# Kernel tuning notes

Hardware: AMD Instinct MI355X
Metric: run time of the kernel (lower is better)

The kernel has to match this reference:

```python
import jax, jax.numpy as jnp
import numpy as np
import math

B, C, H, W = 4, 256, 64, 64
NUM_HEADS = 4
GROUPS = 32
EPS = 1e-5


def setup_inputs() -> dict:
    key = jax.random.key(0)
    ks = jax.random.split(key, 7)
    x = jax.random.normal(ks[0], (B, C, H, W), dtype=jnp.float32)
    gn_w = jax.random.normal(ks[1], (C,), dtype=jnp.float32) * 0.02 + 1.0
    gn_b = jax.random.normal(ks[2], (C,), dtype=jnp.float32) * 0.02
    qkv_w = jax.random.normal(ks[3], (3 * C, C), dtype=jnp.float32) * (1.0 / math.sqrt(C))
    qkv_b = jax.random.normal(ks[4], (3 * C,), dtype=jnp.float32) * 0.02
    proj_w = jax.random.normal(ks[5], (C, C), dtype=jnp.float32) * (1.0 / math.sqrt(C))
    proj_b = jax.random.normal(ks[6], (C,), dtype=jnp.float32) * 0.02
    return {"x": x, "gn_w": gn_w, "gn_b": gn_b, "qkv_w": qkv_w,
            "qkv_b": qkv_b, "proj_w": proj_w, "proj_b": proj_b}


def reference(x, gn_w, gn_b, qkv_w, qkv_b, proj_w, proj_b):
    b, c, h, w = x.shape
    t = h * w
    xf = x.reshape(b, c, t)                       # [B, C, T]

    # GroupNorm(32, C) over (channels-in-group, T)
    xg = xf.reshape(b, GROUPS, c // GROUPS, t)
    mean = jnp.mean(xg, axis=(2, 3), keepdims=True)
    var = jnp.var(xg, axis=(2, 3), keepdims=True)
    xn = ((xg - mean) * jax.lax.rsqrt(var + EPS)).reshape(b, c, t)
    xn = xn * gn_w[None, :, None] + gn_b[None, :, None]

    # 1x1 conv QKV: [B, 3C, T]
    qkv = jnp.einsum('oc,bct->bot', qkv_w, xn) + qkv_b[None, :, None]

    nh = NUM_HEADS
    ch = c // nh
    q, k, v = jnp.split(qkv, 3, axis=1)           # each [B, H*ch, T]
    q = q.reshape(b * nh, ch, t)
    k = k.reshape(b * nh, ch, t)
    v = v.reshape(b * nh, ch, t)

    scale = 1.0 / math.sqrt(math.sqrt(ch))
    logits = jnp.einsum('bct,bcs->bts', q * scale, k * scale)   # [B*H, T, T]
    weight = jax.nn.softmax(logits.astype(jnp.float32), axis=-1).astype(logits.dtype)
    a = jnp.einsum('bts,bcs->bct', weight, v)     # [B*H, ch, T]
    a = a.reshape(b, c, t)

    hproj = jnp.einsum('oc,bct->bot', proj_w, a) + proj_b[None, :, None]
    return (xf + hproj).reshape(b, c, h, w)
```

## Files before the change

### kernel.cpp

```cpp
#include <hip/hip_runtime.h>
#include <cstdint>
#include <cstddef>

#define TT 4096
#define CCH 256

typedef __attribute__((ext_vector_type(8))) short short8;
typedef __attribute__((ext_vector_type(4))) float f32x4;
typedef __attribute__((ext_vector_type(4))) unsigned int u32x4;

__device__ __forceinline__ unsigned short f2bf(float f){
  unsigned int x = __float_as_uint(f);
  x += 0x7fffu + ((x >> 16) & 1u);
  return (unsigned short)(x >> 16);
}
__device__ __forceinline__ int sw(int row, int col){
  return (row << 6) + ((((col >> 3) ^ (row & 7)) << 3)) + (col & 7);
}
__device__ __forceinline__ void pl16(unsigned &a, unsigned &b){
  asm("v_permlane16_swap_b32 %0, %1" : "+v"(a), "+v"(b));
}
__device__ __forceinline__ void pl32(unsigned &a, unsigned &b){
  asm("v_permlane32_swap_b32 %0, %1" : "+v"(a), "+v"(b));
}
__device__ __forceinline__ unsigned cvt_pk_bf16(float lo, float hi){
  unsigned r;
  asm("v_cvt_pk_bf16_f32 %0, %1, %2" : "=v"(r) : "v"(lo), "v"(hi));
  return r;
}

__global__ __launch_bounds__(256)
void wconv_gn(const float* __restrict__ qkv_w, const float* __restrict__ proj_w,
              const float* __restrict__ x,
              unsigned short* __restrict__ wq_bf, unsigned short* __restrict__ wp_bf,
              float* __restrict__ stats){
  int bid = blockIdx.x, tid = threadIdx.x;
  if (bid < 256){
    const float* src = (bid < 192) ? qkv_w : proj_w;
    unsigned short* dst = (bid < 192) ? wq_bf : wp_bf;
    int i = (bid < 192 ? bid : bid - 192) * 256 + tid;
    float4 u = *(const float4*)(src + (size_t)i * 4);
    ushort4 r; r.x = f2bf(u.x); r.y = f2bf(u.y); r.z = f2bf(u.z); r.w = f2bf(u.w);
    *(ushort4*)(dst + (size_t)i * 4) = r;
    return;
  }
  int sg = bid - 256;
  const float4* p = (const float4*)(x + (size_t)sg * 32768);
  float s = 0.f, sq = 0.f;
  #pragma unroll
  for (int it = 0; it < 32; ++it){
    float4 u = p[it * 256 + tid];
    s  += u.x + u.y + u.z + u.w;
    sq += u.x*u.x + u.y*u.y + u.z*u.z + u.w*u.w;
  }
  #pragma unroll
  for (int off = 32; off >= 1; off >>= 1){
    s  += __shfl_down(s, off);
    sq += __shfl_down(sq, off);
  }
  __shared__ float ls[4], lq[4];
  int w_ = tid >> 6, lane = tid & 63;
  if (lane == 0){ ls[w_] = s; lq[w_] = sq; }
  __syncthreads();
  if (tid == 0){
    float S = ls[0]+ls[1]+ls[2]+ls[3];
    float Q = lq[0]+lq[1]+lq[2]+lq[3];
    float mean = S * (1.f/32768.f);
    float var  = Q * (1.f/32768.f) - mean*mean;
    stats[2*sg]   = mean;
    stats[2*sg+1] = rsqrtf(var + 1e-5f);
  }
}

__global__ __launch_bounds__(256)
void gn_apply_t(const float* __restrict__ x, const float* __restrict__ gw,
                const float* __restrict__ gb, const float* __restrict__ stats,
                unsigned short* __restrict__ xnT){
  __shared__ unsigned short t_lds[64][72];
  int tid = threadIdx.x;
  int t0 = blockIdx.x << 6, c0 = blockIdx.y << 6, b = blockIdx.z;
  int t4 = (tid & 15) << 2, cr = tid >> 4;
  #pragma unroll
  for (int pass = 0; pass < 4; ++pass){
    int cl = (pass << 4) + cr;
    int c = c0 + cl;
    int sg = (b << 5) | (c >> 3);
    float mean = stats[2*sg], rstd = stats[2*sg+1];
    float sc = gw[c] * rstd;
    float sh = gb[c] - mean * sc;
    float4 u = *(const float4*)(x + ((size_t)(b*CCH + c))*TT + t0 + t4);
    t_lds[t4+0][cl] = f2bf(u.x*sc + sh);
    t_lds[t4+1][cl] = f2bf(u.y*sc + sh);
    t_lds[t4+2][cl] = f2bf(u.z*sc + sh);
    t_lds[t4+3][cl] = f2bf(u.w*sc + sh);
  }
  __syncthreads();
  #pragma unroll
  for (int pass = 0; pass < 2; ++pass){
    int chunk = (pass << 8) + tid;
    int row = chunk >> 3, c8 = (chunk & 7) << 3;
    *(uint4*)(xnT + ((size_t)b*TT + t0 + row)*256 + c0 + c8) = *(const uint4*)&t_lds[row][c8];
  }
}

__global__ __launch_bounds__(256)
void qkv_mfma(const unsigned short* __restrict__ wb, const float* __restrict__ bias,
              const unsigned short* __restrict__ xnT,
              unsigned short* __restrict__ qT, unsigned short* __restrict__ kT,
              unsigned short* __restrict__ vO){
  __shared__ unsigned short x_lds[4096];
  int tid = threadIdx.x;
  int w = tid >> 6, lane = tid & 63, quad = lane >> 4, l15 = lane & 15;
  int t0 = blockIdx.x << 6, o0 = blockIdx.y << 6, b = blockIdx.z;
  const unsigned short* xb = xnT + (size_t)b * TT * 256;
  const unsigned short* wrow = wb + (size_t)(o0 + (w << 4) + l15) * 256;
  f32x4 acc[4];
  #pragma unroll
  for (int nt = 0; nt < 4; ++nt) acc[nt] = (f32x4){0.f,0.f,0.f,0.f};
  for (int ks = 0; ks < 4; ++ks){
    int k0 = ks << 6;
    __syncthreads();
    #pragma unroll
    for (int pass = 0; pass < 2; ++pass){
      int chunk = (pass << 8) + tid;
      int row = chunk >> 3, c8 = (chunk & 7) << 3;
      *(uint4*)&x_lds[sw(row, c8)] = *(const uint4*)(xb + (size_t)(t0 + row)*256 + k0 + c8);
    }
    __syncthreads();
    short8 wa0 = *(const short8*)(wrow + k0 + (quad << 3));
    short8 wa1 = *(const short8*)(wrow + k0 + 32 + (quad << 3));
    #pragma unroll
    for (int nt = 0; nt < 4; ++nt){
      short8 xb0 = *(const short8*)&x_lds[sw((nt << 4) + l15, quad << 3)];
      short8 xb1 = *(const short8*)&x_lds[sw((nt << 4) + l15, 32 + (quad << 3))];
      acc[nt] = __builtin_amdgcn_mfma_f32_16x16x32_bf16(wa0, xb0, acc[nt], 0, 0, 0);
      acc[nt] = __builtin_amdgcn_mfma_f32_16x16x32_bf16(wa1, xb1, acc[nt], 0, 0, 0);
    }
  }
  int sec = blockIdx.y >> 2, h = blockIdx.y & 3, bh = (b << 2) | h;
  float bs[4];
  #pragma unroll
  for (int r = 0; r < 4; ++r) bs[r] = bias[o0 + (w << 4) + (quad << 2) + r];
  __syncthreads();
  if (sec < 2){
    float qsc = (sec == 0) ? 0.125f * 1.44269504f : 1.0f;
    #pragma unroll
    for (int nt = 0; nt < 4; ++nt){
      ushort4 pk;
      pk.x = f2bf((acc[nt][0] + bs[0]) * qsc);
      pk.y = f2bf((acc[nt][1] + bs[1]) * qsc);
      pk.z = f2bf((acc[nt][2] + bs[2]) * qsc);
      pk.w = f2bf((acc[nt][3] + bs[3]) * qsc);
      *(ushort4*)&x_lds[sw((nt << 4) + l15, (w << 4) + (quad << 2))] = pk;
    }
    __syncthreads();
    unsigned short* dst = (sec == 0) ? qT : kT;
    #pragma unroll
    for (int pass = 0; pass < 2; ++pass){
      int chunk = (pass << 8) + tid;
      int row = chunk >> 3, c8 = (chunk & 7) << 3;
      *(uint4*)(dst + ((size_t)bh*TT + t0 + row)*64 + c8) = *(const uint4*)&x_lds[sw(row, c8)];
    }
  } else {
    #pragma unroll
    for (int nt = 0; nt < 4; ++nt)
      #pragma unroll
      for (int r = 0; r < 4; ++r)
        x_lds[sw((w << 4) + (quad << 2) + r, (nt << 4) + l15)] = f2bf(acc[nt][r] + bs[r]);
    __syncthreads();
    #pragma unroll
    for (int pass = 0; pass < 2; ++pass){
      int chunk = (pass << 8) + tid;
      int row = chunk >> 3, c8 = (chunk & 7) << 3;
      *(uint4*)(vO + ((size_t)bh*64 + row)*TT + t0 + c8) = *(const uint4*)&x_lds[sw(row, c8)];
    }
  }
}

__global__ __launch_bounds__(256, 4)
void attn10(const unsigned short* __restrict__ qT, const unsigned short* __restrict__ kT,
            const unsigned short* __restrict__ vO,
            float* __restrict__ oP, float* __restrict__ lP){
  __shared__ __align__(16) unsigned short k_lds[4096];
  __shared__ __align__(16) unsigned short v_lds[4096];
  int tid = threadIdx.x;
  int w = tid >> 6, lane = tid & 63, quad = lane >> 4, l15 = lane & 15;
  int bh = blockIdx.x & 15;
  int sh = (blockIdx.x >> 4) & 1;
  int tb = blockIdx.x >> 5;
  int t0 = tb << 7;
  const unsigned short* qg = qT + (size_t)bh * TT * 64;
  const unsigned short* kg = kT + (size_t)bh * TT * 64;
  const unsigned short* vg = vO + (size_t)bh * 64 * TT;
  int sbase = sh << 11;

  int row0 = tid >> 3, c80 = (tid & 7) << 3;
  int row1 = row0 + 32;
  int soff0 = sw(row0, c80), soff1 = sw(row1, c80);

  short8 qf[2][2];
  #pragma unroll
  for (int tt2 = 0; tt2 < 2; ++tt2)
    #pragma unroll
    for (int h = 0; h < 2; ++h)
      qf[tt2][h] = *(const short8*)(qg + (size_t)(t0 + (w<<5) + (tt2<<4) + l15)*64 + (h<<5) + (quad<<3));

  short8 ones;
  #pragma unroll
  for (int i = 0; i < 8; ++i) ones[i] = (short)0x3F80;

  f32x4 o_acc[2][4];
  #pragma unroll
  for (int tt2 = 0; tt2 < 2; ++tt2)
    #pragma unroll
    for (int ct = 0; ct < 4; ++ct) o_acc[tt2][ct] = (f32x4){0.f,0.f,0.f,0.f};
  float l_[2] = {0.f, 0.f};

  uint4 kr0 = *(const uint4*)(kg + (size_t)(sbase + row0)*64 + c80);
  uint4 kr1 = *(const uint4*)(kg + (size_t)(sbase + row1)*64 + c80);
  uint4 vr0 = *(const uint4*)(vg + (size_t)row0*TT + sbase + c80);
  uint4 vr1 = *(const uint4*)(vg + (size_t)row1*TT + sbase + c80);

  for (int st = 0; st < 32; ++st){
    __syncthreads();
    *(uint4*)&k_lds[soff0] = kr0;
    *(uint4*)&k_lds[soff1] = kr1;
    *(uint4*)&v_lds[soff0] = vr0;
    *(uint4*)&v_lds[soff1] = vr1;
    if (st < 31){
      int sn = sbase + ((st + 1) << 6);
      kr0 = *(const uint4*)(kg + (size_t)(sn + row0)*64 + c80);
      kr1 = *(const uint4*)(kg + (size_t)(sn + row1)*64 + c80);
      vr0 = *(const uint4*)(vg + (size_t)row0*TT + sn + c80);
      vr1 = *(const uint4*)(vg + (size_t)row1*TT + sn + c80);
    }
    __syncthreads();
    short8 pb[2][2];
    __builtin_amdgcn_s_setprio(1);
    #pragma unroll
    for (int h = 0; h < 2; ++h){
      short8 kae0 = *(const short8*)&k_lds[sw((h << 5) + l15, quad << 3)];
      short8 kae1 = *(const short8*)&k_lds[sw((h << 5) + l15, 32 + (quad << 3))];
      short8 kao0 = *(const short8*)&k_lds[sw((h << 5) + 16 + l15, quad << 3)];
      short8 kao1 = *(const short8*)&k_lds[sw((h << 5) + 16 + l15, 32 + (quad << 3))];
      #pragma unroll
      for (int tt2 = 0; tt2 < 2; ++tt2){
        f32x4 ze = (f32x4){-16.f, -16.f, -16.f, -16.f};
        f32x4 zo = ze;
        ze = __builtin_amdgcn_mfma_f32_16x16x32_bf16(kae0, qf[tt2][0], ze, 0, 0, 0);
        ze = __builtin_amdgcn_mfma_f32_16x16x32_bf16(kae1, qf[tt2][1], ze, 0, 0, 0);
        zo = __builtin_amdgcn_mfma_f32_16x16x32_bf16(kao0, qf[tt2][0], zo, 0, 0, 0);
        zo = __builtin_amdgcn_mfma_f32_16x16x32_bf16(kao1, qf[tt2][1], zo, 0, 0, 0);
        unsigned A0 = cvt_pk_bf16(exp2f(ze[0]), exp2f(ze[1]));
        unsigned A1 = cvt_pk_bf16(exp2f(ze[2]), exp2f(ze[3]));
        unsigned B0 = cvt_pk_bf16(exp2f(zo[0]), exp2f(zo[1]));
        unsigned B1 = cvt_pk_bf16(exp2f(zo[2]), exp2f(zo[3]));
        pl32(A0, B0); pl16(A0, B0);
        pl32(A1, B1); pl16(A1, B1);
        union { u32x4 u; short8 s; } pu;
        pu.u = (u32x4){A0, A1, B0, B1};
        pb[tt2][h] = pu.s;
      }
    }
    #pragma unroll
    for (int tt2 = 0; tt2 < 2; ++tt2){
      f32x4 ls4 = (f32x4){0.f,0.f,0.f,0.f};
      ls4 = __builtin_amdgcn_mfma_f32_16x16x32_bf16(ones, pb[tt2][0], ls4, 0, 0, 0);
      ls4 = __builtin_amdgcn_mfma_f32_16x16x32_bf16(ones, pb[tt2][1], ls4, 0, 0, 0);
      l_[tt2] += ls4[0];
    }
    #pragma unroll
    for (int ct = 0; ct < 4; ++ct){
      short8 va0 = *(const short8*)&v_lds[sw((ct << 4) + l15, quad << 3)];
      short8 va1 = *(const short8*)&v_lds[sw((ct << 4) + l15, 32 + (quad << 3))];
      #pragma unroll
      for (int tt2 = 0; tt2 < 2; ++tt2){
        o_acc[tt2][ct] = __builtin_amdgcn_mfma_f32_16x16x32_bf16(va0, pb[tt2][0], o_acc[tt2][ct], 0, 0, 0);
        o_acc[tt2][ct] = __builtin_amdgcn_mfma_f32_16x16x32_bf16(va1, pb[tt2][1], o_acc[tt2][ct], 0, 0, 0);
      }
    }
    __builtin_amdgcn_s_setprio(0);
  }
  int bid2 = (tb << 4) | bh;
  size_t fb = (size_t)sh * (512*8192) + (size_t)bid2 * 8192;
  #pragma unroll
  for (int tt2 = 0; tt2 < 2; ++tt2)
    #pragma unroll
    for (int ct = 0; ct < 4; ++ct)
      *(f32x4*)(oP + fb + (size_t)((((tt2 << 2) + ct) << 8) + tid) * 4) = o_acc[tt2][ct];
  if (quad == 0){
    #pragma unroll
    for (int tt2 = 0; tt2 < 2; ++tt2)
      lP[((sh << 4) + bh) * 4096 + t0 + (w << 5) + (tt2 << 4) + l15] = l_[tt2];
  }
}

__global__ __launch_bounds__(256)
void attn_comb(const float* __restrict__ oP, const float* __restrict__ lP,
               unsigned short* __restrict__ aT){
  __shared__ __align__(16) unsigned short p_lds[8192];
  int tid = threadIdx.x;
  int w = tid >> 6, lane = tid & 63, quad = lane >> 4, l15 = lane & 15;
  int bh = blockIdx.x & 15, tb = blockIdx.x >> 4;
  int t0 = tb << 7;
  size_t fb = (size_t)blockIdx.x * 8192;
  const size_t HALF = (size_t)512 * 8192;
  float ir[2];
  #pragma unroll
  for (int tt2 = 0; tt2 < 2; ++tt2){
    int t = t0 + (w << 5) + (tt2 << 4) + l15;
    ir[tt2] = 1.f / (lP[bh*4096 + t] + lP[(16 + bh)*4096 + t]);
  }
  #pragma unroll
  for (int tt2 = 0; tt2 < 2; ++tt2)
    #pragma unroll
    for (int ct = 0; ct < 4; ++ct){
      size_t off = fb + (size_t)((((tt2 << 2) + ct) << 8) + tid) * 4;
      f32x4 a = *(const f32x4*)(oP + off);
      f32x4 b = *(const f32x4*)(oP + HALF + off);
      ushort4 ok;
      ok.x = f2bf((a[0] + b[0]) * ir[tt2]);
      ok.y = f2bf((a[1] + b[1]) * ir[tt2]);
      ok.z = f2bf((a[2] + b[2]) * ir[tt2]);
      ok.w = f2bf((a[3] + b[3]) * ir[tt2]);
      *(ushort4*)&p_lds[sw((w << 5) + (tt2 << 4) + l15, (ct << 4) + (quad << 2))] = ok;
    }
  __syncthreads();
  size_t abase = ((size_t)(bh >> 2)*TT + t0)*256 + (size_t)(bh & 3)*64;
  #pragma unroll
  for (int pass = 0; pass < 4; ++pass){
    int chunk = (pass << 8) + tid;
    int row = chunk >> 3, c8 = (chunk & 7) << 3;
    *(uint4*)(aT + abase + (size_t)row*256 + c8) = *(const uint4*)&p_lds[sw(row, c8)];
  }
}

__global__ __launch_bounds__(256)
void proj_mfma(const unsigned short* __restrict__ wb, const float* __restrict__ bias,
               const unsigned short* __restrict__ aT, const float* __restrict__ x,
               float* __restrict__ out){
  __shared__ unsigned short x_lds[4096];
  int tid = threadIdx.x;
  int w = tid >> 6, lane = tid & 63, quad = lane >> 4, l15 = lane & 15;
  int t0 = blockIdx.x << 6, o0 = blockIdx.y << 6, b = blockIdx.z;
  const unsigned short* xb = aT + (size_t)b * TT * 256;
  const unsigned short* wrow = wb + (size_t)(o0 + (w << 4) + l15) * 256;
  f32x4 acc[4];
  #pragma unroll
  for (int nt = 0; nt < 4; ++nt) acc[nt] = (f32x4){0.f,0.f,0.f,0.f};
  for (int ks = 0; ks < 4; ++ks){
    int k0 = ks << 6;
    __syncthreads();
    #pragma unroll
    for (int pass = 0; pass < 2; ++pass){
      int chunk = (pass << 8) + tid;
      int row = chunk >> 3, c8 = (chunk & 7) << 3;
      *(uint4*)&x_lds[sw(row, c8)] = *(const uint4*)(xb + (size_t)(t0 + row)*256 + k0 + c8);
    }
    __syncthreads();
    short8 wa0 = *(const short8*)(wrow + k0 + (quad << 3));
    short8 wa1 = *(const short8*)(wrow + k0 + 32 + (quad << 3));
    #pragma unroll
    for (int nt = 0; nt < 4; ++nt){
      short8 xb0 = *(const short8*)&x_lds[sw((nt << 4) + l15, quad << 3)];
      short8 xb1 = *(const short8*)&x_lds[sw((nt << 4) + l15, 32 + (quad << 3))];
      acc[nt] = __builtin_amdgcn_mfma_f32_16x16x32_bf16(wa0, xb0, acc[nt], 0, 0, 0);
      acc[nt] = __builtin_amdgcn_mfma_f32_16x16x32_bf16(wa1, xb1, acc[nt], 0, 0, 0);
    }
  }
  #pragma unroll
  for (int r = 0; r < 4; ++r){
    int o = o0 + (w << 4) + (quad << 2) + r;
    float bsv = bias[o];
    #pragma unroll
    for (int nt = 0; nt < 4; ++nt){
      size_t idx = ((size_t)(b*CCH + o))*TT + t0 + (nt << 4) + l15;
      out[idx] = acc[nt][r] + bsv + x[idx];
    }
  }
}

extern "C" void kernel_launch(void* const* d_in, const int* in_sizes, int n_in,
                              void* d_out, int out_size, void* d_ws, size_t ws_size,
                              hipStream_t stream){
  const float* x      = (const float*)d_in[0];
  const float* gn_w   = (const float*)d_in[1];
  const float* gn_b   = (const float*)d_in[2];
  const float* qkv_w  = (const float*)d_in[3];
  const float* qkv_b  = (const float*)d_in[4];
  const float* proj_w = (const float*)d_in[5];
  const float* proj_b = (const float*)d_in[6];
  float* out = (float*)d_out;

  float* stats = (float*)d_ws;
  unsigned short* wq_bf = (unsigned short*)(stats + 1024);
  unsigned short* wp_bf = wq_bf + (size_t)768*256;
  unsigned short* xnT   = wp_bf + (size_t)256*256;
  unsigned short* qT    = xnT + (size_t)4*TT*256;
  unsigned short* kT    = qT  + (size_t)16*TT*64;
  unsigned short* vO    = kT  + (size_t)16*TT*64;
  unsigned short* aT    = vO  + (size_t)16*64*TT;
  float* oP = (float*)(aT + (size_t)16*64*TT);
  float* lP = oP + (size_t)2*512*8192;

  wconv_gn<<<384, 256, 0, stream>>>(qkv_w, proj_w, x, wq_bf, wp_bf, stats);
  gn_apply_t<<<dim3(64, 4, 4), 256, 0, stream>>>(x, gn_w, gn_b, stats, xnT);
  qkv_mfma<<<dim3(64, 12, 4), 256, 0, stream>>>(wq_bf, qkv_b, xnT, qT, kT, vO);
  attn10<<<1024, 256, 0, stream>>>(qT, kT, vO, oP, lP);
  attn_comb<<<512, 256, 0, stream>>>(oP, lP, aT);
  proj_mfma<<<dim3(64, 4, 4), 256, 0, stream>>>(wp_bf, proj_b, aT, x, out);
}
```

Measured before the change: 209.9 us.

## Split attention keys four ways with bf16 partial outputs

The attention kernel now splits the key sequence into four chunks instead of two, doubling the grid to 2048 blocks and halving each block's loop length. It also asks for higher occupancy in the launch bounds. Partial outputs are stored as bf16 instead of fp32, which holds total partial-buffer traffic roughly constant, and the combine kernel sums four partials. The trade-off is more precision loss in the partials and a tighter register budget that could cause spills.

```diff
diff --git a/kernel.cpp b/kernel.cpp
--- a/kernel.cpp
+++ b/kernel.cpp
@@ -13,6 +13,9 @@
   unsigned int x = __float_as_uint(f);
   x += 0x7fffu + ((x >> 16) & 1u);
   return (unsigned short)(x >> 16);
+}
+__device__ __forceinline__ float bf2f(unsigned short u){
+  union { unsigned int i; float f; } v; v.i = ((unsigned int)u) << 16; return v.f;
 }
 __device__ __forceinline__ int sw(int row, int col){
   return (row << 6) + ((((col >> 3) ^ (row & 7)) << 3)) + (col & 7);
@@ -177,22 +180,22 @@
   }
 }
 
-__global__ __launch_bounds__(256, 4)
+__global__ __launch_bounds__(256, 8)
 void attn10(const unsigned short* __restrict__ qT, const unsigned short* __restrict__ kT,
             const unsigned short* __restrict__ vO,
-            float* __restrict__ oP, float* __restrict__ lP){
+            unsigned short* __restrict__ oPb, float* __restrict__ lP){
   __shared__ __align__(16) unsigned short k_lds[4096];
   __shared__ __align__(16) unsigned short v_lds[4096];
   int tid = threadIdx.x;
   int w = tid >> 6, lane = tid & 63, quad = lane >> 4, l15 = lane & 15;
   int bh = blockIdx.x & 15;
-  int sh = (blockIdx.x >> 4) & 1;
-  int tb = blockIdx.x >> 5;
+  int sh = (blockIdx.x >> 4) & 3;
+  int tb = blockIdx.x >> 6;
   int t0 = tb << 7;
   const unsigned short* qg = qT + (size_t)bh * TT * 64;
   const unsigned short* kg = kT + (size_t)bh * TT * 64;
   const unsigned short* vg = vO + (size_t)bh * 64 * TT;
-  int sbase = sh << 11;
+  int sbase = sh << 10;
 
   int row0 = tid >> 3, c80 = (tid & 7) << 3;
   int row1 = row0 + 32;
@@ -221,13 +224,13 @@
   uint4 vr0 = *(const uint4*)(vg + (size_t)row0*TT + sbase + c80);
   uint4 vr1 = *(const uint4*)(vg + (size_t)row1*TT + sbase + c80);
 
-  for (int st = 0; st < 32; ++st){
+  for (int st = 0; st < 16; ++st){
     __syncthreads();
     *(uint4*)&k_lds[soff0] = kr0;
     *(uint4*)&k_lds[soff1] = kr1;
     *(uint4*)&v_lds[soff0] = vr0;
     *(uint4*)&v_lds[soff1] = vr1;
-    if (st < 31){
+    if (st < 15){
       int sn = sbase + ((st + 1) << 6);
       kr0 = *(const uint4*)(kg + (size_t)(sn + row0)*64 + c80);
       kr1 = *(const uint4*)(kg + (size_t)(sn + row1)*64 + c80);
@@ -282,12 +285,16 @@
     __builtin_amdgcn_s_setprio(0);
   }
   int bid2 = (tb << 4) | bh;
-  size_t fb = (size_t)sh * (512*8192) + (size_t)bid2 * 8192;
+  size_t fb = ((size_t)sh * 512 + bid2) * 8192;
   #pragma unroll
   for (int tt2 = 0; tt2 < 2; ++tt2)
     #pragma unroll
-    for (int ct = 0; ct < 4; ++ct)
-      *(f32x4*)(oP + fb + (size_t)((((tt2 << 2) + ct) << 8) + tid) * 4) = o_acc[tt2][ct];
+    for (int ct = 0; ct < 4; ++ct){
+      f32x4 o = o_acc[tt2][ct];
+      ushort4 ob;
+      ob.x = f2bf(o[0]); ob.y = f2bf(o[1]); ob.z = f2bf(o[2]); ob.w = f2bf(o[3]);
+      *(ushort4*)(oPb + fb + (size_t)((((tt2 << 2) + ct) << 8) + tid) * 4) = ob;
+    }
   if (quad == 0){
     #pragma unroll
     for (int tt2 = 0; tt2 < 2; ++tt2)
@@ -296,7 +303,7 @@
 }
 
 __global__ __launch_bounds__(256)
-void attn_comb(const float* __restrict__ oP, const float* __restrict__ lP,
+void attn_comb(const unsigned short* __restrict__ oPb, const float* __restrict__ lP,
                unsigned short* __restrict__ aT){
   __shared__ __align__(16) unsigned short p_lds[8192];
   int tid = threadIdx.x;
@@ -304,25 +311,32 @@
   int bh = blockIdx.x & 15, tb = blockIdx.x >> 4;
   int t0 = tb << 7;
   size_t fb = (size_t)blockIdx.x * 8192;
-  const size_t HALF = (size_t)512 * 8192;
+  const size_t QTR = (size_t)512 * 8192;
   float ir[2];
   #pragma unroll
   for (int tt2 = 0; tt2 < 2; ++tt2){
     int t = t0 + (w << 5) + (tt2 << 4) + l15;
-    ir[tt2] = 1.f / (lP[bh*4096 + t] + lP[(16 + bh)*4096 + t]);
+    float l = 0.f;
+    #pragma unroll
+    for (int q = 0; q < 4; ++q) l += lP[((q << 4) + bh) * 4096 + t];
+    ir[tt2] = 1.f / l;
   }
   #pragma unroll
   for (int tt2 = 0; tt2 < 2; ++tt2)
     #pragma unroll
     for (int ct = 0; ct < 4; ++ct){
       size_t off = fb + (size_t)((((tt2 << 2) + ct) << 8) + tid) * 4;
-      f32x4 a = *(const f32x4*)(oP + off);
-      f32x4 b = *(const f32x4*)(oP + HALF + off);
+      float s0 = 0.f, s1 = 0.f, s2 = 0.f, s3 = 0.f;
+      #pragma unroll
+      for (int q = 0; q < 4; ++q){
+        ushort4 pv = *(const ushort4*)(oPb + q * QTR + off);
+        s0 += bf2f(pv.x); s1 += bf2f(pv.y); s2 += bf2f(pv.z); s3 += bf2f(pv.w);
+      }
       ushort4 ok;
-      ok.x = f2bf((a[0] + b[0]) * ir[tt2]);
-      ok.y = f2bf((a[1] + b[1]) * ir[tt2]);
-      ok.z = f2bf((a[2] + b[2]) * ir[tt2]);
-      ok.w = f2bf((a[3] + b[3]) * ir[tt2]);
+      ok.x = f2bf(s0 * ir[tt2]);
+      ok.y = f2bf(s1 * ir[tt2]);
+      ok.z = f2bf(s2 * ir[tt2]);
+      ok.w = f2bf(s3 * ir[tt2]);
       *(ushort4*)&p_lds[sw((w << 5) + (tt2 << 4) + l15, (ct << 4) + (quad << 2))] = ok;
     }
   __syncthreads();
@@ -400,13 +414,13 @@
   unsigned short* kT    = qT  + (size_t)16*TT*64;
   unsigned short* vO    = kT  + (size_t)16*TT*64;
   unsigned short* aT    = vO  + (size_t)16*64*TT;
-  float* oP = (float*)(aT + (size_t)16*64*TT);
-  float* lP = oP + (size_t)2*512*8192;
+  unsigned short* oPb   = aT + (size_t)16*64*TT;
+  float* lP = (float*)(oPb + (size_t)4*512*8192);
 
   wconv_gn<<<384, 256, 0, stream>>>(qkv_w, proj_w, x, wq_bf, wp_bf, stats);
   gn_apply_t<<<dim3(64, 4, 4), 256, 0, stream>>>(x, gn_w, gn_b, stats, xnT);
   qkv_mfma<<<dim3(64, 12, 4), 256, 0, stream>>>(wq_bf, qkv_b, xnT, qT, kT, vO);
-  attn10<<<1024, 256, 0, stream>>>(qT, kT, vO, oP, lP);
-  attn_comb<<<512, 256, 0, stream>>>(oP, lP, aT);
+  attn10<<<2048, 256, 0, stream>>>(qT, kT, vO, oPb, lP);
+  attn_comb<<<512, 256, 0, stream>>>(oPb, lP, aT);
   proj_mfma<<<dim3(64, 4, 4), 256, 0, stream>>>(wp_bf, proj_b, aT, x, out);
 }
```

Result: slower. 655.4 us (+212.3%).

## Halve query tile per attention block to double grid and raise occupancy

Applied to the files above, without the earlier changes.

The attention kernel now has each wave handle 16 query rows instead of 32, so a block covers 64 query positions and the grid doubles to 2048 blocks. Launch bounds rise to 6 blocks per CU to raise occupancy and latency hiding. The combine kernel and partial-buffer layout are resized to match. In exchange, each K/V tile loaded into LDS is reused across half as many queries, doubling K/V global and LDS traffic per unit of work.

```diff
diff --git a/kernel.cpp b/kernel.cpp
--- a/kernel.cpp
+++ b/kernel.cpp
@@ -177,8 +177,8 @@
   }
 }
 
-__global__ __launch_bounds__(256, 4)
-void attn10(const unsigned short* __restrict__ qT, const unsigned short* __restrict__ kT,
+__global__ __launch_bounds__(256, 6)
+void attn11(const unsigned short* __restrict__ qT, const unsigned short* __restrict__ kT,
             const unsigned short* __restrict__ vO,
             float* __restrict__ oP, float* __restrict__ lP){
   __shared__ __align__(16) unsigned short k_lds[4096];
@@ -188,7 +188,7 @@
   int bh = blockIdx.x & 15;
   int sh = (blockIdx.x >> 4) & 1;
   int tb = blockIdx.x >> 5;
-  int t0 = tb << 7;
+  int t0 = tb << 6;
   const unsigned short* qg = qT + (size_t)bh * TT * 64;
   const unsigned short* kg = kT + (size_t)bh * TT * 64;
   const unsigned short* vg = vO + (size_t)bh * 64 * TT;
@@ -198,23 +198,18 @@
   int row1 = row0 + 32;
   int soff0 = sw(row0, c80), soff1 = sw(row1, c80);
 
-  short8 qf[2][2];
-  #pragma unroll
-  for (int tt2 = 0; tt2 < 2; ++tt2)
-    #pragma unroll
-    for (int h = 0; h < 2; ++h)
-      qf[tt2][h] = *(const short8*)(qg + (size_t)(t0 + (w<<5) + (tt2<<4) + l15)*64 + (h<<5) + (quad<<3));
+  short8 qf[2];
+  qf[0] = *(const short8*)(qg + (size_t)(t0 + (w << 4) + l15)*64 + (quad << 3));
+  qf[1] = *(const short8*)(qg + (size_t)(t0 + (w << 4) + l15)*64 + 32 + (quad << 3));
 
   short8 ones;
   #pragma unroll
   for (int i = 0; i < 8; ++i) ones[i] = (short)0x3F80;
 
-  f32x4 o_acc[2][4];
-  #pragma unroll
-  for (int tt2 = 0; tt2 < 2; ++tt2)
-    #pragma unroll
-    for (int ct = 0; ct < 4; ++ct) o_acc[tt2][ct] = (f32x4){0.f,0.f,0.f,0.f};
-  float l_[2] = {0.f, 0.f};
+  f32x4 o_acc[4];
+  #pragma unroll
+  for (int ct = 0; ct < 4; ++ct) o_acc[ct] = (f32x4){0.f,0.f,0.f,0.f};
+  float l_ = 0.f;
 
   uint4 kr0 = *(const uint4*)(kg + (size_t)(sbase + row0)*64 + c80);
   uint4 kr1 = *(const uint4*)(kg + (size_t)(sbase + row1)*64 + c80);
@@ -235,7 +230,7 @@
       vr1 = *(const uint4*)(vg + (size_t)row1*TT + sn + c80);
     }
     __syncthreads();
-    short8 pb[2][2];
+    short8 pb[2];
     __builtin_amdgcn_s_setprio(1);
     #pragma unroll
     for (int h = 0; h < 2; ++h){
@@ -243,92 +238,72 @@
       short8 kae1 = *(const short8*)&k_lds[sw((h << 5) + l15, 32 + (quad << 3))];
       short8 kao0 = *(const short8*)&k_lds[sw((h << 5) + 16 + l15, quad << 3)];
       short8 kao1 = *(const short8*)&k_lds[sw((h << 5) + 16 + l15, 32 + (quad << 3))];
-      #pragma unroll
-      for (int tt2 = 0; tt2 < 2; ++tt2){
-        f32x4 ze = (f32x4){-16.f, -16.f, -16.f, -16.f};
-        f32x4 zo = ze;
-        ze = __builtin_amdgcn_mfma_f32_16x16x32_bf16(kae0, qf[tt2][0], ze, 0, 0, 0);
-        ze = __builtin_amdgcn_mfma_f32_16x16x32_bf16(kae1, qf[tt2][1], ze, 0, 0, 0);
-        zo = __builtin_amdgcn_mfma_f32_16x16x32_bf16(kao0, qf[tt2][0], zo, 0, 0, 0);
-        zo = __builtin_amdgcn_mfma_f32_16x16x32_bf16(kao1, qf[tt2][1], zo, 0, 0, 0);
-        unsigned A0 = cvt_pk_bf16(exp2f(ze[0]), exp2f(ze[1]));
-        unsigned A1 = cvt_pk_bf16(exp2f(ze[2]), exp2f(ze[3]));
-        unsigned B0 = cvt_pk_bf16(exp2f(zo[0]), exp2f(zo[1]));
-        unsigned B1 = cvt_pk_bf16(exp2f(zo[2]), exp2f(zo[3]));
-        pl32(A0, B0); pl16(A0, B0);
-        pl32(A1, B1); pl16(A1, B1);
-        union { u32x4 u; short8 s; } pu;
-        pu.u = (u32x4){A0, A1, B0, B1};
-        pb[tt2][h] = pu.s;
-      }
-    }
-    #pragma unroll
-    for (int tt2 = 0; tt2 < 2; ++tt2){
-      f32x4 ls4 = (f32x4){0.f,0.f,0.f,0.f};
-      ls4 = __builtin_amdgcn_mfma_f32_16x16x32_bf16(ones, pb[tt2][0], ls4, 0, 0, 0);
-      ls4 = __builtin_amdgcn_mfma_f32_16x16x32_bf16(ones, pb[tt2][1], ls4, 0, 0, 0);
-      l_[tt2] += ls4[0];
-    }
+      f32x4 ze = (f32x4){-16.f, -16.f, -16.f, -16.f};
+      f32x4 zo = ze;
+      ze = __builtin_amdgcn_mfma_f32_16x16x32_bf16(kae0, qf[0], ze, 0, 0, 0);
+      ze = __builtin_amdgcn_mfma_f32_16x16x32_bf16(kae1, qf[1], ze, 0, 0, 0);
+      zo = __builtin_amdgcn_mfma_f32_16x16x32_bf16(kao0, qf[0], zo, 0, 0, 0);
+      zo = __builtin_amdgcn_mfma_f32_16x16x32_bf16(kao1, qf[1], zo, 0, 0, 0);
+      unsigned A0 = cvt_pk_bf16(exp2f(ze[0]), exp2f(ze[1]));
+      unsigned A1 = cvt_pk_bf16(exp2f(ze[2]), exp2f(ze[3]));
+      unsigned B0 = cvt_pk_bf16(exp2f(zo[0]), exp2f(zo[1]));
+      unsigned B1 = cvt_pk_bf16(exp2f(zo[2]), exp2f(zo[3]));
+      pl32(A0, B0); pl16(A0, B0);
+      pl32(A1, B1); pl16(A1, B1);
+      union { u32x4 u; short8 s; } pu;
+      pu.u = (u32x4){A0, A1, B0, B1};
+      pb[h] = pu.s;
+    }
+    f32x4 ls4 = (f32x4){0.f,0.f,0.f,0.f};
+    ls4 = __builtin_amdgcn_mfma_f32_16x16x32_bf16(ones, pb[0], ls4, 0, 0, 0);
+    ls4 = __builtin_amdgcn_mfma_f32_16x16x32_bf16(ones, pb[1], ls4, 0, 0, 0);
+    l_ += ls4[0];
     #pragma unroll
     for (int ct = 0; ct < 4; ++ct){
       short8 va0 = *(const short8*)&v_lds[sw((ct << 4) + l15, quad << 3)];
       short8 va1 = *(const short8*)&v_lds[sw((ct << 4) + l15, 32 + (quad << 3))];
-      #pragma unroll
-      for (int tt2 = 0; tt2 < 2; ++tt2){
-        o_acc[tt2][ct] = __builtin_amdgcn_mfma_f32_16x16x32_bf16(va0, pb[tt2][0], o_acc[tt2][ct], 0, 0, 0);
-        o_acc[tt2][ct] = __builtin_amdgcn_mfma_f32_16x16x32_bf16(va1, pb[tt2][1], o_acc[tt2][ct], 0, 0, 0);
-      }
+      o_acc[ct] = __builtin_amdgcn_mfma_f32_16x16x32_bf16(va0, pb[0], o_acc[ct], 0, 0, 0);
+      o_acc[ct] = __builtin_amdgcn_mfma_f32_16x16x32_bf16(va1, pb[1], o_acc[ct], 0, 0, 0);
     }
     __builtin_amdgcn_s_setprio(0);
   }
   int bid2 = (tb << 4) | bh;
-  size_t fb = (size_t)sh * (512*8192) + (size_t)bid2 * 8192;
-  #pragma unroll
-  for (int tt2 = 0; tt2 < 2; ++tt2)
-    #pragma unroll
-    for (int ct = 0; ct < 4; ++ct)
-      *(f32x4*)(oP + fb + (size_t)((((tt2 << 2) + ct) << 8) + tid) * 4) = o_acc[tt2][ct];
-  if (quad == 0){
-    #pragma unroll
-    for (int tt2 = 0; tt2 < 2; ++tt2)
-      lP[((sh << 4) + bh) * 4096 + t0 + (w << 5) + (tt2 << 4) + l15] = l_[tt2];
-  }
+  size_t fb = ((size_t)sh * 1024 + bid2) * 4096;
+  #pragma unroll
+  for (int ct = 0; ct < 4; ++ct)
+    *(f32x4*)(oP + fb + (size_t)(((ct << 8) + tid) * 4)) = o_acc[ct];
+  if (quad == 0)
+    lP[((sh << 4) + bh) * 4096 + t0 + (w << 4) + l15] = l_;
 }
 
 __global__ __launch_bounds__(256)
 void attn_comb(const float* __restrict__ oP, const float* __restrict__ lP,
                unsigned short* __restrict__ aT){
-  __shared__ __align__(16) unsigned short p_lds[8192];
+  __shared__ __align__(16) unsigned short p_lds[4096];
   int tid = threadIdx.x;
   int w = tid >> 6, lane = tid & 63, quad = lane >> 4, l15 = lane & 15;
   int bh = blockIdx.x & 15, tb = blockIdx.x >> 4;
-  int t0 = tb << 7;
-  size_t fb = (size_t)blockIdx.x * 8192;
-  const size_t HALF = (size_t)512 * 8192;
-  float ir[2];
-  #pragma unroll
-  for (int tt2 = 0; tt2 < 2; ++tt2){
-    int t = t0 + (w << 5) + (tt2 << 4) + l15;
-    ir[tt2] = 1.f / (lP[bh*4096 + t] + lP[(16 + bh)*4096 + t]);
-  }
-  #pragma unroll
-  for (int tt2 = 0; tt2 < 2; ++tt2)
-    #pragma unroll
-    for (int ct = 0; ct < 4; ++ct){
-      size_t off = fb + (size_t)((((tt2 << 2) + ct) << 8) + tid) * 4;
-      f32x4 a = *(const f32x4*)(oP + off);
-      f32x4 b = *(const f32x4*)(oP + HALF + off);
-      ushort4 ok;
-      ok.x = f2bf((a[0] + b[0]) * ir[tt2]);
-      ok.y = f2bf((a[1] + b[1]) * ir[tt2]);
-      ok.z = f2bf((a[2] + b[2]) * ir[tt2]);
-      ok.w = f2bf((a[3] + b[3]) * ir[tt2]);
-      *(ushort4*)&p_lds[sw((w << 5) + (tt2 << 4) + l15, (ct << 4) + (quad << 2))] = ok;
-    }
+  int t0 = tb << 6;
+  size_t fb = (size_t)blockIdx.x * 4096;
+  const size_t HALF = (size_t)1024 * 4096;
+  int t = t0 + (w << 4) + l15;
+  float ir = 1.f / (lP[bh*4096 + t] + lP[(16 + bh)*4096 + t]);
+  #pragma unroll
+  for (int ct = 0; ct < 4; ++ct){
+    size_t off = fb + (size_t)(((ct << 8) + tid) * 4);
+    f32x4 a = *(const f32x4*)(oP + off);
+    f32x4 b = *(const f32x4*)(oP + HALF + off);
+    ushort4 ok;
+    ok.x = f2bf((a[0] + b[0]) * ir);
+    ok.y = f2bf((a[1] + b[1]) * ir);
+    ok.z = f2bf((a[2] + b[2]) * ir);
+    ok.w = f2bf((a[3] + b[3]) * ir);
+    *(ushort4*)&p_lds[sw((w << 4) + l15, (ct << 4) + (quad << 2))] = ok;
+  }
   __syncthreads();
   size_t abase = ((size_t)(bh >> 2)*TT + t0)*256 + (size_t)(bh & 3)*64;
   #pragma unroll
-  for (int pass = 0; pass < 4; ++pass){
+  for (int pass = 0; pass < 2; ++pass){
     int chunk = (pass << 8) + tid;
     int row = chunk >> 3, c8 = (chunk & 7) << 3;
     *(uint4*)(aT + abase + (size_t)row*256 + c8) = *(const uint4*)&p_lds[sw(row, c8)];
@@ -401,12 +376,12 @@
   unsigned short* vO    = kT  + (size_t)16*TT*64;
   unsigned short* aT    = vO  + (size_t)16*64*TT;
   float* oP = (float*)(aT + (size_t)16*64*TT);
-  float* lP = oP + (size_t)2*512*8192;
+  float* lP = oP + (size_t)2*1024*4096;
 
   wconv_gn<<<384, 256, 0, stream>>>(qkv_w, proj_w, x, wq_bf, wp_bf, stats);
   gn_apply_t<<<dim3(64, 4, 4), 256, 0, stream>>>(x, gn_w, gn_b, stats, xnT);
   qkv_mfma<<<dim3(64, 12, 4), 256, 0, stream>>>(wq_bf, qkv_b, xnT, qT, kT, vO);
-  attn10<<<1024, 256, 0, stream>>>(qT, kT, vO, oP, lP);
-  attn_comb<<<512, 256, 0, stream>>>(oP, lP, aT);
+  attn11<<<2048, 256, 0, stream>>>(qT, kT, vO, oP, lP);
+  attn_comb<<<1024, 256, 0, stream>>>(oP, lP, aT);
   proj_mfma<<<dim3(64, 4, 4), 256, 0, stream>>>(wp_bf, proj_b, aT, x, out);
 }
```

Result: slower. 327.4 us (+56.0%).
